# Performance work log

Hardware: AMD Instinct MI355X
Metric: run time of the kernel (lower is better)

Reference implementation:

```python
import jax, jax.numpy as jnp
import numpy as np

N, E, D = 50000, 800000, 128
BN_EPS = 1e-5
COORDS_WEIGHT = 1.0


def _p(key, shape, scale=0.05):
    return (jax.random.normal(key, shape, dtype=jnp.float32) * scale)


def setup_inputs() -> dict:
    key = jax.random.key(0)
    ks = jax.random.split(key, 16)
    inp = {
        "h": jax.random.normal(ks[0], (N, D), dtype=jnp.float32),
        "coord": jax.random.normal(ks[1], (N, 3), dtype=jnp.float32),
        "edge_index": jax.random.randint(ks[2], (2, E), 0, N, dtype=jnp.int32),
        # edge_mlp: Linear(2D+1 -> D), BN, ReLU, Linear(D -> D), BN, ReLU
        "e_w1": _p(ks[3], (D, 2 * D + 1)), "e_b1": jnp.zeros((D,), jnp.float32),
        "e_g1": jnp.ones((D,), jnp.float32), "e_be1": jnp.zeros((D,), jnp.float32),
        "e_w2": _p(ks[4], (D, D)), "e_b2": jnp.zeros((D,), jnp.float32),
        "e_g2": jnp.ones((D,), jnp.float32), "e_be2": jnp.zeros((D,), jnp.float32),
        # node_mlp: Linear(D + D -> D), BN, ReLU, Linear(D -> D)
        "n_w1": _p(ks[5], (D, 2 * D)), "n_b1": jnp.zeros((D,), jnp.float32),
        "n_g1": jnp.ones((D,), jnp.float32), "n_be1": jnp.zeros((D,), jnp.float32),
        "n_w2": _p(ks[6], (D, D)), "n_b2": jnp.zeros((D,), jnp.float32),
        # coord_mlp: Linear(D -> D), BN, ReLU, Linear(D -> 1, bias=False, tiny init)
        "c_w1": _p(ks[7], (D, D)), "c_b1": jnp.zeros((D,), jnp.float32),
        "c_g1": jnp.ones((D,), jnp.float32), "c_be1": jnp.zeros((D,), jnp.float32),
        "c_w2": _p(ks[8], (1, D), scale=0.001),
    }
    return inp


def _bn(x, g, b):
    # BatchNorm1d in training mode: biased batch stats over dim 0
    m = jnp.mean(x, axis=0)
    v = jnp.var(x, axis=0)
    return (x - m) * jax.lax.rsqrt(v + BN_EPS) * g + b


def _segment_mean(data, seg, num_segments):
    s = jax.ops.segment_sum(data, seg, num_segments=num_segments)
    c = jax.ops.segment_sum(jnp.ones((data.shape[0], 1), data.dtype), seg,
                            num_segments=num_segments)
    return s / jnp.maximum(c, 1.0)


def reference(h, coord, edge_index,
              e_w1, e_b1, e_g1, e_be1, e_w2, e_b2, e_g2, e_be2,
              n_w1, n_b1, n_g1, n_be1, n_w2, n_b2,
              c_w1, c_b1, c_g1, c_be1, c_w2):
    row, col = edge_index[0], edge_index[1]
    # coord2radial
    coord_diff = coord[row] - coord[col]                      # [E,3]
    radial = jnp.sum(coord_diff ** 2, axis=1, keepdims=True)  # [E,1]
    # edge_model
    e_in = jnp.concatenate([h[row], h[col], radial], axis=1)  # [E, 2D+1]
    x = jax.nn.relu(_bn(e_in @ e_w1.T + e_b1, e_g1, e_be1))
    edge_feat = jax.nn.relu(_bn(x @ e_w2.T + e_b2, e_g2, e_be2))  # [E,D]
    # coord_model
    y = jax.nn.relu(_bn(edge_feat @ c_w1.T + c_b1, c_g1, c_be1))
    scale = y @ c_w2.T                                        # [E,1]
    trans = jnp.clip(coord_diff * scale, -100.0, 100.0)
    coord_out = coord + _segment_mean(trans, row, coord.shape[0]) * COORDS_WEIGHT
    # node_model
    agg = _segment_mean(edge_feat, row, h.shape[0])           # [N,D]
    n_in = jnp.concatenate([h, agg], axis=1)                  # [N,2D]
    z = jax.nn.relu(_bn(n_in @ n_w1.T + n_b1, n_g1, n_be1))
    h_out = h + (z @ n_w2.T + n_b2)                           # recurrent residual
    return (h_out, coord_out)
```

## Files before the change

kernel.cpp:

```cpp
#include <hip/hip_runtime.h>

#define Nn 50000
#define En 800000
#define NSLOT 64

typedef __attribute__((ext_vector_type(8))) short short8;
typedef __attribute__((ext_vector_type(4))) float f32x4;

union U8 { uint4 u4; unsigned short us[8]; short8 s8; };

static __device__ __forceinline__ float bf2f(unsigned int lo16) {
  return __uint_as_float(lo16 << 16);
}
static __device__ __forceinline__ unsigned short f2bf(float f) {
  unsigned int x = __float_as_uint(f);
  return (unsigned short)((x + 0x7FFFu + ((x >> 16) & 1u)) >> 16);
}


__global__ __launch_bounds__(256) void k_prep_h(const float* __restrict__ h,
                                                unsigned short* __restrict__ nodeA) {
  int idx = blockIdx.x * 256 + threadIdx.x;
  if (idx >= Nn * 128) return;
  int n = idx >> 7, k = idx & 127;
  nodeA[(size_t)n * 256 + k] = f2bf(h[idx]);
}

__global__ __launch_bounds__(256) void k_prep_w(const float* __restrict__ src,
                                                unsigned short* __restrict__ dst, int Ksrc,
                                                int koff, int kshift, int total) {
  int idx = blockIdx.x * 256 + threadIdx.x;
  if (idx >= total) return;
  int n = idx >> kshift;
  int k = idx & ((1 << kshift) - 1);
  dst[idx] = f2bf(src[n * Ksrc + koff + k]);
}

__global__ void k_wlast(const float* __restrict__ e_w1, float* __restrict__ wlast) {
  int t = threadIdx.x;
  if (t < 128) wlast[t] = e_w1[t * 257 + 256];
}


__global__ __launch_bounds__(256) void k_count(const int* __restrict__ row, int* __restrict__ cnt) {
  int e = blockIdx.x * 256 + threadIdx.x;
  atomicAdd(&cnt[row[e]], 1);
}

__global__ __launch_bounds__(256) void k_fill(const int* __restrict__ row, int* __restrict__ cursor,
                                              int* __restrict__ elist) {
  int e = blockIdx.x * 256 + threadIdx.x;
  int pos = atomicAdd(&cursor[row[e]], 1);
  elist[pos] = e;
}

__global__ __launch_bounds__(1024) void k_scan(const int* __restrict__ cnt, int* __restrict__ start,
                                               int* __restrict__ cursor, int n) {
  __shared__ int wsum[16];
  __shared__ int carry;
  int tid = threadIdx.x, lane = tid & 63, wid = tid >> 6;
  if (tid == 0) carry = 0;
  __syncthreads();
  for (int base = 0; base < n; base += 1024) {
    int i = base + tid;
    int v = (i < n) ? cnt[i] : 0;
    int x = v;
#pragma unroll
    for (int d = 1; d < 64; d <<= 1) {
      int y = __shfl_up(x, d, 64);
      if (lane >= d) x += y;
    }
    if (lane == 63) wsum[wid] = x;
    __syncthreads();
    if (wid == 0) {
      int s = (lane < 16) ? wsum[lane] : 0;
#pragma unroll
      for (int d = 1; d < 16; d <<= 1) {
        int y = __shfl_up(s, d, 64);
        if (lane >= d) s += y;
      }
      if (lane < 16) wsum[lane] = s;
    }
    __syncthreads();
    int c0 = carry;
    int waveoff = (wid > 0) ? wsum[wid - 1] : 0;
    int incl = c0 + waveoff + x;
    if (i < n) {
      start[i] = incl - v;
      cursor[i] = incl - v;
    }
    __syncthreads();
    if (tid == 1023) carry = incl;
    __syncthreads();
  }
}


__global__ void k_fin(const float* __restrict__ statS, const float* __restrict__ statQ,
                      const float* __restrict__ g, const float* __restrict__ be, float invR,
                      float* __restrict__ bnS, float* __restrict__ bnSh) {
  int c = threadIdx.x;
  if (c >= 128) return;
  float s = 0.f, q = 0.f;
  for (int k = 0; k < NSLOT; ++k) {
    s += statS[k * 128 + c];
    q += statQ[k * 128 + c];
  }
  float mean = s * invR;
  float var = fmaxf(q * invR - mean * mean, 0.f);
  float rs = rsqrtf(var + 1e-5f);
  float sc = g[c] * rs;
  bnS[c] = sc;
  bnSh[c] = be[c] - mean * sc;
}

template <int KSTEPS, bool BN_A, bool STATS, bool FP32OUT>
__global__ __launch_bounds__(256) void k_gemmW(
    const unsigned short* __restrict__ A, int Astride ,
    const unsigned short* __restrict__ W , const float* __restrict__ bias,
    const float* __restrict__ bnS, const float* __restrict__ bnSh,
    unsigned short* __restrict__ outb, float* __restrict__ statS, float* __restrict__ statQ,
    const float* __restrict__ hres, float* __restrict__ outf, int R) {
  constexpr int K = KSTEPS * 32;
  constexpr int WST = K + 8;
  constexpr int SEGS = K / 8;
  __shared__ __align__(16) unsigned short smem[128 * WST];
  __shared__ float ssum[4][128], ssq[4][128];
  int tid = threadIdx.x;
  int w = tid >> 6, lane = tid & 63, m = lane & 15, kq = lane >> 4;
  int rbase = blockIdx.x * 128;
#pragma unroll
  for (int it = 0; it < SEGS / 2; ++it) {
    int idx = it * 256 + tid;
    int n = idx / SEGS, seg = idx % SEGS;
    uint4 v = *(const uint4*)(W + (size_t)n * K + seg * 8);
    *(uint4*)(smem + n * WST + seg * 8) = v;
  }
  __syncthreads();
  int row0 = rbase + w * 32 + m;
  int rc0 = min(row0, R - 1);
  int rc1 = min(row0 + 16, R - 1);
  f32x4 acc[2][8];
#pragma unroll
  for (int rt = 0; rt < 2; ++rt)
#pragma unroll
    for (int c = 0; c < 8; ++c) acc[rt][c] = (f32x4){0.f, 0.f, 0.f, 0.f};
#pragma unroll
  for (int ks = 0; ks < KSTEPS; ++ks) {
    int k0 = ks * 32 + kq * 8;
    U8 ua0, ua1;
    ua0.u4 = *(const uint4*)(A + (size_t)rc0 * Astride + k0);
    ua1.u4 = *(const uint4*)(A + (size_t)rc1 * Astride + k0);
    if (BN_A) {
      const float4* sp = (const float4*)(bnS + k0);
      const float4* hp = (const float4*)(bnSh + k0);
      float4 s0 = sp[0], s1 = sp[1], h0 = hp[0], h1 = hp[1];
      float sv[8] = {s0.x, s0.y, s0.z, s0.w, s1.x, s1.y, s1.z, s1.w};
      float hv[8] = {h0.x, h0.y, h0.z, h0.w, h1.x, h1.y, h1.z, h1.w};
#pragma unroll
      for (int j = 0; j < 8; ++j) {
        ua0.us[j] = f2bf(fmaxf(bf2f(ua0.us[j]) * sv[j] + hv[j], 0.f));
        ua1.us[j] = f2bf(fmaxf(bf2f(ua1.us[j]) * sv[j] + hv[j], 0.f));
      }
    }
#pragma unroll
    for (int c = 0; c < 8; ++c) {
      U8 ub;
      ub.u4 = *(const uint4*)(smem + (c * 16 + m) * WST + k0);
      acc[0][c] = __builtin_amdgcn_mfma_f32_16x16x32_bf16(ua0.s8, ub.s8, acc[0][c], 0, 0, 0);
      acc[1][c] = __builtin_amdgcn_mfma_f32_16x16x32_bf16(ua1.s8, ub.s8, acc[1][c], 0, 0, 0);
    }
  }
  if constexpr (FP32OUT) {
#pragma unroll
    for (int rt = 0; rt < 2; ++rt)
#pragma unroll
      for (int c = 0; c < 8; ++c) {
        int n = c * 16 + m;
        float bn_ = bias[n];
#pragma unroll
        for (int j = 0; j < 4; ++j) {
          int rr = rbase + w * 32 + rt * 16 + kq * 4 + j;
          if (rr < R) {
            size_t o = (size_t)rr * 128 + n;
            outf[o] = acc[rt][c][j] + bn_ + hres[o];
          }
        }
      }
  } else {
    __syncthreads();
    unsigned short* tile = smem;
#pragma unroll
    for (int c = 0; c < 8; ++c) {
      int n = c * 16 + m;
      float bn_ = bias ? bias[n] : 0.f;
      float s = 0.f, q = 0.f;
#pragma unroll
      for (int rt = 0; rt < 2; ++rt)
#pragma unroll
        for (int j = 0; j < 4; ++j) {
          int lr = w * 32 + rt * 16 + kq * 4 + j;
          float v = acc[rt][c][j] + bn_;
          tile[lr * 136 + n] = f2bf(v);
          if (STATS) {
            float sv = (rbase + lr < R) ? v : 0.f;
            s += sv;
            q = fmaf(sv, sv, q);
          }
        }
      if (STATS) {
        s += __shfl_xor(s, 16, 64); s += __shfl_xor(s, 32, 64);
        q += __shfl_xor(q, 16, 64); q += __shfl_xor(q, 32, 64);
        if (kq == 0) { ssum[w][n] = s; ssq[w][n] = q; }
      }
    }
    __syncthreads();
    const uint4* tl = (const uint4*)tile;
#pragma unroll
    for (int u = 0; u < 8; ++u) {
      int idx = u * 256 + tid;
      int rr = idx >> 4, seg = idx & 15;
      if (rbase + rr < R)
        *(uint4*)(outb + (size_t)(rbase + rr) * 128 + seg * 8) = tl[rr * 17 + seg];
    }
    if (STATS && tid < 128) {
      float s = ssum[0][tid] + ssum[1][tid] + ssum[2][tid] + ssum[3][tid];
      float q = ssq[0][tid] + ssq[1][tid] + ssq[2][tid] + ssq[3][tid];
      int slot = blockIdx.x & (NSLOT - 1);
      atomicAdd(&statS[slot * 128 + tid], s);
      atomicAdd(&statQ[slot * 128 + tid], q);
    }
  }
}

__global__ __launch_bounds__(256) void k_edge_comb(
    const unsigned short* __restrict__ hWr, const unsigned short* __restrict__ hWc,
    const float* __restrict__ coord, const int* __restrict__ rowp, const int* __restrict__ colp,
    const float* __restrict__ wlast, unsigned short* __restrict__ t,
    float* __restrict__ statS, float* __restrict__ statQ, int nwaves) {
  int tid = threadIdx.x, lane = tid & 63;
  int wid = blockIdx.x * 4 + (tid >> 6);
  int c2 = lane * 2;
  float wl0 = wlast[c2], wl1 = wlast[c2 + 1];
  float s0 = 0.f, s1 = 0.f, q0 = 0.f, q1 = 0.f;
  for (int e = wid; e < En; e += nwaves) {
    int r = rowp[e], c = colp[e];
    float dx = coord[r * 3 + 0] - coord[c * 3 + 0];
    float dy = coord[r * 3 + 1] - coord[c * 3 + 1];
    float dz = coord[r * 3 + 2] - coord[c * 3 + 2];
    float rad = dx * dx + dy * dy + dz * dz;
    unsigned int ua = *(const unsigned int*)(hWr + (size_t)r * 128 + c2);
    unsigned int ub = *(const unsigned int*)(hWc + (size_t)c * 128 + c2);
    float v0 = bf2f(ua & 0xFFFFu) + bf2f(ub & 0xFFFFu) + rad * wl0;
    float v1 = bf2f(ua >> 16) + bf2f(ub >> 16) + rad * wl1;
    *(unsigned int*)(t + (size_t)e * 128 + c2) = (unsigned)f2bf(v0) | ((unsigned)f2bf(v1) << 16);
    s0 += v0; q0 = fmaf(v0, v0, q0);
    s1 += v1; q1 = fmaf(v1, v1, q1);
  }
  int slot = wid & (NSLOT - 1);
  atomicAdd(&statS[slot * 128 + c2], s0);
  atomicAdd(&statS[slot * 128 + c2 + 1], s1);
  atomicAdd(&statQ[slot * 128 + c2], q0);
  atomicAdd(&statQ[slot * 128 + c2 + 1], q1);
}


__global__ __launch_bounds__(256) void k_scale(const unsigned short* __restrict__ t,
                                               const float* __restrict__ bnS,
                                               const float* __restrict__ bnSh,
                                               const float* __restrict__ cw2,
                                               float* __restrict__ scaleE) {
  int tid = threadIdx.x;
  int lane = tid & 63;
  long e = (long)blockIdx.x * 4 + (tid >> 6);
  int c2 = lane * 2;
  unsigned int u = *(const unsigned int*)(t + e * 128 + c2);
  float v0 = fmaxf(bf2f(u & 0xFFFFu) * bnS[c2] + bnSh[c2], 0.f);
  float v1 = fmaxf(bf2f(u >> 16) * bnS[c2 + 1] + bnSh[c2 + 1], 0.f);
  float p = v0 * cw2[c2] + v1 * cw2[c2 + 1];
#pragma unroll
  for (int d = 32; d; d >>= 1) p += __shfl_xor(p, d, 64);
  if (lane == 0) scaleE[e] = p;
}

__global__ __launch_bounds__(256) void k_agg(const unsigned short* __restrict__ t,
                                             const int* __restrict__ elist,
                                             const int* __restrict__ start,
                                             const int* __restrict__ cnt,
                                             const float* __restrict__ bnS,
                                             const float* __restrict__ bnSh,
                                             unsigned short* __restrict__ nodeA) {
  int tid = threadIdx.x;
  int lane = tid & 63;
  int n = blockIdx.x * 4 + (tid >> 6);
  if (n >= Nn) return;
  int deg = cnt[n], off = start[n];
  int c2 = lane * 2;
  float s0 = bnS[c2], s1 = bnS[c2 + 1], h0 = bnSh[c2], h1 = bnSh[c2 + 1];
  float a0 = 0.f, a1 = 0.f;
  for (int j = 0; j < deg; ++j) {
    int e = elist[off + j];
    unsigned int u = *(const unsigned int*)(t + (size_t)e * 128 + c2);
    a0 += fmaxf(bf2f(u & 0xFFFFu) * s0 + h0, 0.f);
    a1 += fmaxf(bf2f(u >> 16) * s1 + h1, 0.f);
  }
  float inv = 1.f / fmaxf((float)deg, 1.f);
  unsigned int o = (unsigned)f2bf(a0 * inv) | ((unsigned)f2bf(a1 * inv) << 16);
  *(unsigned int*)(nodeA + (size_t)n * 256 + 128 + c2) = o;
}

__global__ __launch_bounds__(256) void k_coord(const float* __restrict__ coord,
                                               const int* __restrict__ col,
                                               const int* __restrict__ elist,
                                               const int* __restrict__ start,
                                               const int* __restrict__ cnt,
                                               const float* __restrict__ scaleE,
                                               float* __restrict__ cout) {
  int tid = threadIdx.x;
  int lane = tid & 63;
  int n = blockIdx.x * 4 + (tid >> 6);
  if (n >= Nn) return;
  int deg = cnt[n], off = start[n];
  float cx0 = coord[n * 3 + 0], cy0 = coord[n * 3 + 1], cz0 = coord[n * 3 + 2];
  float ax = 0.f, ay = 0.f, az = 0.f;
  for (int j = lane; j < deg; j += 64) {
    int e = elist[off + j];
    int c = col[e];
    float s = scaleE[e];
    float tx = (cx0 - coord[c * 3 + 0]) * s;
    float ty = (cy0 - coord[c * 3 + 1]) * s;
    float tz = (cz0 - coord[c * 3 + 2]) * s;
    ax += fminf(fmaxf(tx, -100.f), 100.f);
    ay += fminf(fmaxf(ty, -100.f), 100.f);
    az += fminf(fmaxf(tz, -100.f), 100.f);
  }
#pragma unroll
  for (int d = 32; d; d >>= 1) {
    ax += __shfl_xor(ax, d, 64);
    ay += __shfl_xor(ay, d, 64);
    az += __shfl_xor(az, d, 64);
  }
  if (lane == 0) {
    float inv = 1.f / fmaxf((float)deg, 1.f);
    cout[n * 3 + 0] = cx0 + ax * inv;
    cout[n * 3 + 1] = cy0 + ay * inv;
    cout[n * 3 + 2] = cz0 + az * inv;
  }
}


extern "C" void kernel_launch(void* const* d_in, const int* in_sizes, int n_in, void* d_out,
                              int out_size, void* d_ws, size_t ws_size, hipStream_t stream) {
  (void)in_sizes; (void)n_in; (void)out_size; (void)ws_size;
  const float* h = (const float*)d_in[0];
  const float* coord = (const float*)d_in[1];
  const int* eidx = (const int*)d_in[2];
  const int* row = eidx;
  const int* col = eidx + En;
  const float* e_w1 = (const float*)d_in[3];
  const float* e_b1 = (const float*)d_in[4];
  const float* e_g1 = (const float*)d_in[5];
  const float* e_be1 = (const float*)d_in[6];
  const float* e_w2 = (const float*)d_in[7];
  const float* e_b2 = (const float*)d_in[8];
  const float* e_g2 = (const float*)d_in[9];
  const float* e_be2 = (const float*)d_in[10];
  const float* n_w1 = (const float*)d_in[11];
  const float* n_b1 = (const float*)d_in[12];
  const float* n_g1 = (const float*)d_in[13];
  const float* n_be1 = (const float*)d_in[14];
  const float* n_w2 = (const float*)d_in[15];
  const float* n_b2 = (const float*)d_in[16];
  const float* c_w1 = (const float*)d_in[17];
  const float* c_b1 = (const float*)d_in[18];
  const float* c_g1 = (const float*)d_in[19];
  const float* c_be1 = (const float*)d_in[20];
  const float* c_w2 = (const float*)d_in[21];

  char* base = (char*)d_ws;
  size_t off = 0;
  auto alloc = [&](size_t bytes) -> void* {
    void* p = base + off;
    off = (off + bytes + 255) & ~(size_t)255;
    return p;
  };
  unsigned short* t = (unsigned short*)alloc((size_t)En * 128 * 2);
  unsigned short* nodeA = (unsigned short*)alloc((size_t)Nn * 256 * 2);
  unsigned short* hWr = (unsigned short*)alloc((size_t)Nn * 128 * 2);
  unsigned short* hWc = (unsigned short*)alloc((size_t)Nn * 128 * 2);
  float* scaleE = (float*)alloc((size_t)En * 4);
  int* cnt = (int*)alloc((size_t)Nn * 4);
  int* startp = (int*)alloc((size_t)Nn * 4);
  int* cursor = (int*)alloc((size_t)Nn * 4);
  int* elist = (int*)alloc((size_t)En * 4);
  float* statS = (float*)alloc(4 * NSLOT * 128 * 4);
  float* statQ = (float*)alloc(4 * NSLOT * 128 * 4);
  float* bnS = (float*)alloc(4 * 128 * 4);
  float* bnSh = (float*)alloc(4 * 128 * 4);
  unsigned short* w1a = (unsigned short*)alloc(128 * 128 * 2);
  unsigned short* w1b = (unsigned short*)alloc(128 * 128 * 2);
  unsigned short* w2b = (unsigned short*)alloc(128 * 128 * 2);
  unsigned short* c1b = (unsigned short*)alloc(128 * 128 * 2);
  unsigned short* n1b = (unsigned short*)alloc(128 * 256 * 2);
  unsigned short* n2b = (unsigned short*)alloc(128 * 128 * 2);
  float* wlast = (float*)alloc(128 * 4);

  hipMemsetAsync(cnt, 0, (size_t)Nn * 4, stream);
  hipMemsetAsync(statS, 0, 4 * NSLOT * 128 * 4, stream);
  hipMemsetAsync(statQ, 0, 4 * NSLOT * 128 * 4, stream);

  k_prep_h<<<(Nn * 128 + 255) / 256, 256, 0, stream>>>(h, nodeA);
  k_prep_w<<<(128 * 128 + 255) / 256, 256, 0, stream>>>(e_w1, w1a, 257, 0, 7, 128 * 128);
  k_prep_w<<<(128 * 128 + 255) / 256, 256, 0, stream>>>(e_w1, w1b, 257, 128, 7, 128 * 128);
  k_prep_w<<<(128 * 128 + 255) / 256, 256, 0, stream>>>(e_w2, w2b, 128, 0, 7, 128 * 128);
  k_prep_w<<<(128 * 128 + 255) / 256, 256, 0, stream>>>(c_w1, c1b, 128, 0, 7, 128 * 128);
  k_prep_w<<<(128 * 256 + 255) / 256, 256, 0, stream>>>(n_w1, n1b, 256, 0, 8, 128 * 256);
  k_prep_w<<<(128 * 128 + 255) / 256, 256, 0, stream>>>(n_w2, n2b, 128, 0, 7, 128 * 128);
  k_wlast<<<1, 128, 0, stream>>>(e_w1, wlast);

  k_count<<<En / 256, 256, 0, stream>>>(row, cnt);
  k_scan<<<1, 1024, 0, stream>>>(cnt, startp, cursor, Nn);
  k_fill<<<En / 256, 256, 0, stream>>>(row, cursor, elist);

  const int gridN = (Nn + 127) / 128;
  k_gemmW<4, false, false, false><<<gridN, 256, 0, stream>>>(
      nodeA, 256, w1a, e_b1, nullptr, nullptr, hWr, nullptr, nullptr, nullptr, nullptr, Nn);
  k_gemmW<4, false, false, false><<<gridN, 256, 0, stream>>>(
      nodeA, 256, w1b, nullptr, nullptr, nullptr, hWc, nullptr, nullptr, nullptr, nullptr, Nn);

  k_edge_comb<<<1280, 256, 0, stream>>>(hWr, hWc, coord, row, col, wlast, t,
                                        statS + 0 * NSLOT * 128, statQ + 0 * NSLOT * 128,
                                        1280 * 4);
  k_fin<<<1, 128, 0, stream>>>(statS + 0 * NSLOT * 128, statQ + 0 * NSLOT * 128, e_g1, e_be1,
                               1.f / En, bnS + 0, bnSh + 0);

  k_gemmW<4, true, true, false><<<En / 128, 256, 0, stream>>>(
      t, 128, w2b, e_b2, bnS + 0, bnSh + 0, t, statS + 1 * NSLOT * 128, statQ + 1 * NSLOT * 128,
      nullptr, nullptr, En);
  k_fin<<<1, 128, 0, stream>>>(statS + 1 * NSLOT * 128, statQ + 1 * NSLOT * 128, e_g2, e_be2,
                               1.f / En, bnS + 128, bnSh + 128);

  k_agg<<<(Nn + 3) / 4, 256, 0, stream>>>(t, elist, startp, cnt, bnS + 128, bnSh + 128, nodeA);

  k_gemmW<4, true, true, false><<<En / 128, 256, 0, stream>>>(
      t, 128, c1b, c_b1, bnS + 128, bnSh + 128, t, statS + 2 * NSLOT * 128,
      statQ + 2 * NSLOT * 128, nullptr, nullptr, En);
  k_fin<<<1, 128, 0, stream>>>(statS + 2 * NSLOT * 128, statQ + 2 * NSLOT * 128, c_g1, c_be1,
                               1.f / En, bnS + 256, bnSh + 256);

  k_scale<<<En / 4, 256, 0, stream>>>(t, bnS + 256, bnSh + 256, c_w2, scaleE);
  float* hout = (float*)d_out;
  float* cout = hout + (size_t)Nn * 128;
  k_coord<<<(Nn + 3) / 4, 256, 0, stream>>>(coord, col, elist, startp, cnt, scaleE, cout);

  k_gemmW<8, false, true, false><<<gridN, 256, 0, stream>>>(
      nodeA, 256, n1b, n_b1, nullptr, nullptr, t, statS + 3 * NSLOT * 128,
      statQ + 3 * NSLOT * 128, nullptr, nullptr, Nn);
  k_fin<<<1, 128, 0, stream>>>(statS + 3 * NSLOT * 128, statQ + 3 * NSLOT * 128, n_g1, n_be1,
                               1.f / Nn, bnS + 384, bnSh + 384);
  k_gemmW<4, true, false, true><<<gridN, 256, 0, stream>>>(
      t, 128, n2b, n_b2, bnS + 384, bnSh + 384, nullptr, nullptr, nullptr, h, hout, Nn);
}
```

Measured before the change: 897.0 us.

## Sort edges by row, recompute first edge layer in GEMM, fuse coord MLP with aggregation

```diff
diff --git a/kernel.cpp b/kernel.cpp
--- a/kernel.cpp
+++ b/kernel.cpp
@@ -47,11 +47,16 @@
   atomicAdd(&cnt[row[e]], 1);
 }
 
-__global__ __launch_bounds__(256) void k_fill(const int* __restrict__ row, int* __restrict__ cursor,
-                                              int* __restrict__ elist) {
+__global__ __launch_bounds__(256) void k_fill(const int* __restrict__ row,
+                                              const int* __restrict__ col,
+                                              int* __restrict__ cursor,
+                                              unsigned short* __restrict__ rowS,
+                                              unsigned short* __restrict__ colS) {
   int e = blockIdx.x * 256 + threadIdx.x;
-  int pos = atomicAdd(&cursor[row[e]], 1);
-  elist[pos] = e;
+  int r = row[e];
+  int pos = atomicAdd(&cursor[r], 1);
+  rowS[pos] = (unsigned short)r;
+  colS[pos] = (unsigned short)col[e];
 }
 
 __global__ __launch_bounds__(1024) void k_scan(const int* __restrict__ cnt, int* __restrict__ start,
@@ -114,10 +119,10 @@
   bnSh[c] = be[c] - mean * sc;
 }
 
-template <int KSTEPS, bool BN_A, bool STATS, bool FP32OUT>
+template <int KSTEPS, bool BN_A, bool STATS, bool FP32OUT, bool STORE>
 __global__ __launch_bounds__(256) void k_gemmW(
-    const unsigned short* __restrict__ A, int Astride ,
-    const unsigned short* __restrict__ W , const float* __restrict__ bias,
+    const unsigned short* __restrict__ A, int Astride,
+    const unsigned short* __restrict__ W, const float* __restrict__ bias,
     const float* __restrict__ bnS, const float* __restrict__ bnSh,
     unsigned short* __restrict__ outb, float* __restrict__ statS, float* __restrict__ statQ,
     const float* __restrict__ hres, float* __restrict__ outf, int R) {
@@ -188,7 +193,7 @@
         }
       }
   } else {
-    __syncthreads();
+    if constexpr (STORE) __syncthreads();
     unsigned short* tile = smem;
 #pragma unroll
     for (int c = 0; c < 8; ++c) {
@@ -201,7 +206,7 @@
         for (int j = 0; j < 4; ++j) {
           int lr = w * 32 + rt * 16 + kq * 4 + j;
           float v = acc[rt][c][j] + bn_;
-          tile[lr * 136 + n] = f2bf(v);
+          if (STORE) tile[lr * 136 + n] = f2bf(v);
           if (STATS) {
             float sv = (rbase + lr < R) ? v : 0.f;
             s += sv;
@@ -214,46 +219,54 @@
         if (kq == 0) { ssum[w][n] = s; ssq[w][n] = q; }
       }
     }
-    __syncthreads();
-    const uint4* tl = (const uint4*)tile;
-#pragma unroll
-    for (int u = 0; u < 8; ++u) {
-      int idx = u * 256 + tid;
-      int rr = idx >> 4, seg = idx & 15;
-      if (rbase + rr < R)
-        *(uint4*)(outb + (size_t)(rbase + rr) * 128 + seg * 8) = tl[rr * 17 + seg];
-    }
-    if (STATS && tid < 128) {
-      float s = ssum[0][tid] + ssum[1][tid] + ssum[2][tid] + ssum[3][tid];
-      float q = ssq[0][tid] + ssq[1][tid] + ssq[2][tid] + ssq[3][tid];
-      int slot = blockIdx.x & (NSLOT - 1);
-      atomicAdd(&statS[slot * 128 + tid], s);
-      atomicAdd(&statQ[slot * 128 + tid], q);
-    }
-  }
-}
-
-__global__ __launch_bounds__(256) void k_edge_comb(
+    if constexpr (STORE) {
+      __syncthreads();
+      const uint4* tl = (const uint4*)tile;
+#pragma unroll
+      for (int u = 0; u < 8; ++u) {
+        int idx = u * 256 + tid;
+        int rr = idx >> 4, seg = idx & 15;
+        if (rbase + rr < R)
+          *(uint4*)(outb + (size_t)(rbase + rr) * 128 + seg * 8) = tl[rr * 17 + seg];
+      }
+    }
+    if (STATS) {
+      __syncthreads();
+      if (tid < 128) {
+        float s = ssum[0][tid] + ssum[1][tid] + ssum[2][tid] + ssum[3][tid];
+        float q = ssq[0][tid] + ssq[1][tid] + ssq[2][tid] + ssq[3][tid];
+        int slot = blockIdx.x & (NSLOT - 1);
+        atomicAdd(&statS[slot * 128 + tid], s);
+        atomicAdd(&statQ[slot * 128 + tid], q);
+      }
+    }
+  }
+}
+
+__global__ __launch_bounds__(256) void k_stats1(
     const unsigned short* __restrict__ hWr, const unsigned short* __restrict__ hWc,
-    const float* __restrict__ coord, const int* __restrict__ rowp, const int* __restrict__ colp,
-    const float* __restrict__ wlast, unsigned short* __restrict__ t,
-    float* __restrict__ statS, float* __restrict__ statQ, int nwaves) {
+    const float* __restrict__ coord, const unsigned short* __restrict__ rowS,
+    const unsigned short* __restrict__ colS, const float* __restrict__ wlast,
+    float* __restrict__ radS, float* __restrict__ statS, float* __restrict__ statQ,
+    int per_wave) {
   int tid = threadIdx.x, lane = tid & 63;
   int wid = blockIdx.x * 4 + (tid >> 6);
+  int e0 = wid * per_wave;
+  int e1 = min(e0 + per_wave, En);
   int c2 = lane * 2;
   float wl0 = wlast[c2], wl1 = wlast[c2 + 1];
   float s0 = 0.f, s1 = 0.f, q0 = 0.f, q1 = 0.f;
-  for (int e = wid; e < En; e += nwaves) {
-    int r = rowp[e], c = colp[e];
+  for (int e = e0; e < e1; ++e) {
+    int r = rowS[e], c = colS[e];
     float dx = coord[r * 3 + 0] - coord[c * 3 + 0];
     float dy = coord[r * 3 + 1] - coord[c * 3 + 1];
     float dz = coord[r * 3 + 2] - coord[c * 3 + 2];
     float rad = dx * dx + dy * dy + dz * dz;
+    if (lane == 0) radS[e] = rad;
     unsigned int ua = *(const unsigned int*)(hWr + (size_t)r * 128 + c2);
     unsigned int ub = *(const unsigned int*)(hWc + (size_t)c * 128 + c2);
     float v0 = bf2f(ua & 0xFFFFu) + bf2f(ub & 0xFFFFu) + rad * wl0;
     float v1 = bf2f(ua >> 16) + bf2f(ub >> 16) + rad * wl1;
-    *(unsigned int*)(t + (size_t)e * 128 + c2) = (unsigned)f2bf(v0) | ((unsigned)f2bf(v1) << 16);
     s0 += v0; q0 = fmaf(v0, v0, q0);
     s1 += v1; q1 = fmaf(v1, v1, q1);
   }
@@ -264,54 +277,209 @@
   atomicAdd(&statQ[slot * 128 + c2 + 1], q1);
 }
 
-
-__global__ __launch_bounds__(256) void k_scale(const unsigned short* __restrict__ t,
-                                               const float* __restrict__ bnS,
-                                               const float* __restrict__ bnSh,
-                                               const float* __restrict__ cw2,
-                                               float* __restrict__ scaleE) {
+__global__ __launch_bounds__(256) void k_egemm2(
+    const unsigned short* __restrict__ hWr, const unsigned short* __restrict__ hWc,
+    const float* __restrict__ radS, const unsigned short* __restrict__ rowS,
+    const unsigned short* __restrict__ colS, const unsigned short* __restrict__ W,
+    const float* __restrict__ bias, const float* __restrict__ wlast,
+    const float* __restrict__ bnS1, const float* __restrict__ bnSh1,
+    unsigned short* __restrict__ outb, float* __restrict__ statS, float* __restrict__ statQ) {
+  constexpr int WST = 136;
+  __shared__ __align__(16) unsigned short smem[128 * WST];
+  __shared__ float ssum[4][128], ssq[4][128];
   int tid = threadIdx.x;
-  int lane = tid & 63;
-  long e = (long)blockIdx.x * 4 + (tid >> 6);
-  int c2 = lane * 2;
-  unsigned int u = *(const unsigned int*)(t + e * 128 + c2);
-  float v0 = fmaxf(bf2f(u & 0xFFFFu) * bnS[c2] + bnSh[c2], 0.f);
-  float v1 = fmaxf(bf2f(u >> 16) * bnS[c2 + 1] + bnSh[c2 + 1], 0.f);
-  float p = v0 * cw2[c2] + v1 * cw2[c2 + 1];
-#pragma unroll
-  for (int d = 32; d; d >>= 1) p += __shfl_xor(p, d, 64);
-  if (lane == 0) scaleE[e] = p;
-}
-
-__global__ __launch_bounds__(256) void k_agg(const unsigned short* __restrict__ t,
-                                             const int* __restrict__ elist,
-                                             const int* __restrict__ start,
-                                             const int* __restrict__ cnt,
-                                             const float* __restrict__ bnS,
-                                             const float* __restrict__ bnSh,
-                                             unsigned short* __restrict__ nodeA) {
+  int w = tid >> 6, lane = tid & 63, m = lane & 15, kq = lane >> 4;
+  int rbase = blockIdx.x * 128;
+#pragma unroll
+  for (int it = 0; it < 8; ++it) {
+    int idx = it * 256 + tid;
+    int n = idx >> 4, seg = idx & 15;
+    uint4 v = *(const uint4*)(W + (size_t)n * 128 + seg * 8);
+    *(uint4*)(smem + n * WST + seg * 8) = v;
+  }
+  int rc0 = rbase + w * 32 + m, rc1 = rc0 + 16;
+  int r0 = rowS[rc0], c0 = colS[rc0];
+  int r1 = rowS[rc1], c1 = colS[rc1];
+  float rad0 = radS[rc0], rad1 = radS[rc1];
+  __syncthreads();
+  f32x4 acc[2][8];
+#pragma unroll
+  for (int rt = 0; rt < 2; ++rt)
+#pragma unroll
+    for (int c = 0; c < 8; ++c) acc[rt][c] = (f32x4){0.f, 0.f, 0.f, 0.f};
+#pragma unroll
+  for (int ks = 0; ks < 4; ++ks) {
+    int k0 = ks * 32 + kq * 8;
+    U8 a0r, a0c, a1r, a1c;
+    a0r.u4 = *(const uint4*)(hWr + (size_t)r0 * 128 + k0);
+    a0c.u4 = *(const uint4*)(hWc + (size_t)c0 * 128 + k0);
+    a1r.u4 = *(const uint4*)(hWr + (size_t)r1 * 128 + k0);
+    a1c.u4 = *(const uint4*)(hWc + (size_t)c1 * 128 + k0);
+    const float4* wp = (const float4*)(wlast + k0);
+    const float4* sp = (const float4*)(bnS1 + k0);
+    const float4* hp = (const float4*)(bnSh1 + k0);
+    float4 w0 = wp[0], w1 = wp[1], sA = sp[0], sB = sp[1], hA = hp[0], hB = hp[1];
+    float wv[8] = {w0.x, w0.y, w0.z, w0.w, w1.x, w1.y, w1.z, w1.w};
+    float sv[8] = {sA.x, sA.y, sA.z, sA.w, sB.x, sB.y, sB.z, sB.w};
+    float hv[8] = {hA.x, hA.y, hA.z, hA.w, hB.x, hB.y, hB.z, hB.w};
+    U8 ua0, ua1;
+#pragma unroll
+    for (int j = 0; j < 8; ++j) {
+      float v0 = bf2f(a0r.us[j]) + bf2f(a0c.us[j]) + rad0 * wv[j];
+      float v1 = bf2f(a1r.us[j]) + bf2f(a1c.us[j]) + rad1 * wv[j];
+      ua0.us[j] = f2bf(fmaxf(v0 * sv[j] + hv[j], 0.f));
+      ua1.us[j] = f2bf(fmaxf(v1 * sv[j] + hv[j], 0.f));
+    }
+#pragma unroll
+    for (int c = 0; c < 8; ++c) {
+      U8 ub;
+      ub.u4 = *(const uint4*)(smem + (c * 16 + m) * WST + k0);
+      acc[0][c] = __builtin_amdgcn_mfma_f32_16x16x32_bf16(ua0.s8, ub.s8, acc[0][c], 0, 0, 0);
+      acc[1][c] = __builtin_amdgcn_mfma_f32_16x16x32_bf16(ua1.s8, ub.s8, acc[1][c], 0, 0, 0);
+    }
+  }
+  __syncthreads();
+  unsigned short* tile = smem;
+#pragma unroll
+  for (int c = 0; c < 8; ++c) {
+    int n = c * 16 + m;
+    float bn_ = bias[n];
+    float s = 0.f, q = 0.f;
+#pragma unroll
+    for (int rt = 0; rt < 2; ++rt)
+#pragma unroll
+      for (int j = 0; j < 4; ++j) {
+        int lr = w * 32 + rt * 16 + kq * 4 + j;
+        float v = acc[rt][c][j] + bn_;
+        tile[lr * 136 + n] = f2bf(v);
+        s += v;
+        q = fmaf(v, v, q);
+      }
+    s += __shfl_xor(s, 16, 64); s += __shfl_xor(s, 32, 64);
+    q += __shfl_xor(q, 16, 64); q += __shfl_xor(q, 32, 64);
+    if (kq == 0) { ssum[w][n] = s; ssq[w][n] = q; }
+  }
+  __syncthreads();
+  const uint4* tl = (const uint4*)tile;
+#pragma unroll
+  for (int u = 0; u < 8; ++u) {
+    int idx = u * 256 + tid;
+    int rr = idx >> 4, seg = idx & 15;
+    *(uint4*)(outb + (size_t)(rbase + rr) * 128 + seg * 8) = tl[rr * 17 + seg];
+  }
+  if (tid < 128) {
+    float s = ssum[0][tid] + ssum[1][tid] + ssum[2][tid] + ssum[3][tid];
+    float q = ssq[0][tid] + ssq[1][tid] + ssq[2][tid] + ssq[3][tid];
+    int slot = blockIdx.x & (NSLOT - 1);
+    atomicAdd(&statS[slot * 128 + tid], s);
+    atomicAdd(&statQ[slot * 128 + tid], q);
+  }
+}
+
+__global__ __launch_bounds__(256) void k_c1agg(
+    const unsigned short* __restrict__ t, const unsigned short* __restrict__ W,
+    const float* __restrict__ bias, const float* __restrict__ bnS2,
+    const float* __restrict__ bnSh2, const float* __restrict__ bnS3,
+    const float* __restrict__ bnSh3, const float* __restrict__ cw2,
+    const unsigned short* __restrict__ rowS, float* __restrict__ aggAcc,
+    float* __restrict__ scaleE) {
+  __shared__ __align__(16) unsigned short smw[128 * 128];
+  __shared__ __align__(16) unsigned short ytile[128 * 128];
   int tid = threadIdx.x;
-  int lane = tid & 63;
-  int n = blockIdx.x * 4 + (tid >> 6);
-  if (n >= Nn) return;
-  int deg = cnt[n], off = start[n];
-  int c2 = lane * 2;
-  float s0 = bnS[c2], s1 = bnS[c2 + 1], h0 = bnSh[c2], h1 = bnSh[c2 + 1];
-  float a0 = 0.f, a1 = 0.f;
-  for (int j = 0; j < deg; ++j) {
-    int e = elist[off + j];
-    unsigned int u = *(const unsigned int*)(t + (size_t)e * 128 + c2);
-    a0 += fmaxf(bf2f(u & 0xFFFFu) * s0 + h0, 0.f);
-    a1 += fmaxf(bf2f(u >> 16) * s1 + h1, 0.f);
-  }
-  float inv = 1.f / fmaxf((float)deg, 1.f);
-  unsigned int o = (unsigned)f2bf(a0 * inv) | ((unsigned)f2bf(a1 * inv) << 16);
-  *(unsigned int*)(nodeA + (size_t)n * 256 + 128 + c2) = o;
+  int w = tid >> 6, lane = tid & 63, m = lane & 15, kq = lane >> 4;
+  int rbase = blockIdx.x * 128;
+#pragma unroll
+  for (int it = 0; it < 8; ++it) {
+    int idx = it * 256 + tid;
+    int n = idx >> 4, b = idx & 15;
+    uint4 v = *(const uint4*)(W + (size_t)n * 128 + b * 8);
+    *(uint4*)(smw + n * 128 + ((b ^ (n & 15)) << 3)) = v;
+  }
+  __syncthreads();
+  f32x4 acc[2][8];
+#pragma unroll
+  for (int rt = 0; rt < 2; ++rt)
+#pragma unroll
+    for (int c = 0; c < 8; ++c) acc[rt][c] = (f32x4){0.f, 0.f, 0.f, 0.f};
+  int r0l = w * 32 + m, r1l = r0l + 16;
+#pragma unroll
+  for (int ks = 0; ks < 4; ++ks) {
+    int k0 = ks * 32 + kq * 8;
+    int blk = ks * 4 + kq;
+    U8 ua0, ua1;
+    ua0.u4 = *(const uint4*)(t + (size_t)(rbase + r0l) * 128 + k0);
+    ua1.u4 = *(const uint4*)(t + (size_t)(rbase + r1l) * 128 + k0);
+    const float4* sp = (const float4*)(bnS2 + k0);
+    const float4* hp = (const float4*)(bnSh2 + k0);
+    float4 sA = sp[0], sB = sp[1], hA = hp[0], hB = hp[1];
+    float sv[8] = {sA.x, sA.y, sA.z, sA.w, sB.x, sB.y, sB.z, sB.w};
+    float hv[8] = {hA.x, hA.y, hA.z, hA.w, hB.x, hB.y, hB.z, hB.w};
+#pragma unroll
+    for (int j = 0; j < 8; ++j) {
+      ua0.us[j] = f2bf(fmaxf(bf2f(ua0.us[j]) * sv[j] + hv[j], 0.f));
+      ua1.us[j] = f2bf(fmaxf(bf2f(ua1.us[j]) * sv[j] + hv[j], 0.f));
+    }
+    *(uint4*)(ytile + r0l * 128 + ((blk ^ m) << 3)) = ua0.u4;
+    *(uint4*)(ytile + r1l * 128 + ((blk ^ m) << 3)) = ua1.u4;
+#pragma unroll
+    for (int c = 0; c < 8; ++c) {
+      U8 ub;
+      ub.u4 = *(const uint4*)(smw + (c * 16 + m) * 128 + ((blk ^ m) << 3));
+      acc[0][c] = __builtin_amdgcn_mfma_f32_16x16x32_bf16(ua0.s8, ub.s8, acc[0][c], 0, 0, 0);
+      acc[1][c] = __builtin_amdgcn_mfma_f32_16x16x32_bf16(ua1.s8, ub.s8, acc[1][c], 0, 0, 0);
+    }
+  }
+  float p[2][4] = {{0.f, 0.f, 0.f, 0.f}, {0.f, 0.f, 0.f, 0.f}};
+#pragma unroll
+  for (int c = 0; c < 8; ++c) {
+    int n = c * 16 + m;
+    float b1 = bias[n], s3 = bnS3[n], sh3 = bnSh3[n], w2 = cw2[n];
+#pragma unroll
+    for (int rt = 0; rt < 2; ++rt)
+#pragma unroll
+      for (int j = 0; j < 4; ++j) {
+        float t3v = acc[rt][c][j] + b1;
+        p[rt][j] += w2 * fmaxf(t3v * s3 + sh3, 0.f);
+      }
+  }
+#pragma unroll
+  for (int rt = 0; rt < 2; ++rt)
+#pragma unroll
+    for (int j = 0; j < 4; ++j) {
+      float v = p[rt][j];
+      v += __shfl_xor(v, 1, 64); v += __shfl_xor(v, 2, 64);
+      v += __shfl_xor(v, 4, 64); v += __shfl_xor(v, 8, 64);
+      if (m == 0) scaleE[rbase + w * 32 + rt * 16 + kq * 4 + j] = v;
+    }
+  __syncthreads();
+  int ch = tid & 127, half = tid >> 7;
+  int rlo = half * 64, rhi = rlo + 64;
+  int cur = rowS[rbase + rlo];
+  float run = 0.f;
+  for (int r = rlo; r < rhi; ++r) {
+    int nid = rowS[rbase + r];
+    if (nid != cur) {
+      atomicAdd(&aggAcc[(size_t)cur * 128 + ch], run);
+      run = 0.f;
+      cur = nid;
+    }
+    run += bf2f(ytile[r * 128 + (((ch >> 3) ^ (r & 15)) << 3) + (ch & 7)]);
+  }
+  atomicAdd(&aggAcc[(size_t)cur * 128 + ch], run);
+}
+
+__global__ __launch_bounds__(256) void k_aggfin(const float* __restrict__ aggAcc,
+                                                const int* __restrict__ cnt,
+                                                unsigned short* __restrict__ nodeA) {
+  int idx = blockIdx.x * 256 + threadIdx.x;
+  if (idx >= Nn * 128) return;
+  int n = idx >> 7, ch = idx & 127;
+  float inv = 1.f / fmaxf((float)cnt[n], 1.f);
+  nodeA[(size_t)n * 256 + 128 + ch] = f2bf(aggAcc[idx] * inv);
 }
 
 __global__ __launch_bounds__(256) void k_coord(const float* __restrict__ coord,
-                                               const int* __restrict__ col,
-                                               const int* __restrict__ elist,
+                                               const unsigned short* __restrict__ colS,
                                                const int* __restrict__ start,
                                                const int* __restrict__ cnt,
                                                const float* __restrict__ scaleE,
@@ -324,8 +492,8 @@
   float cx0 = coord[n * 3 + 0], cy0 = coord[n * 3 + 1], cz0 = coord[n * 3 + 2];
   float ax = 0.f, ay = 0.f, az = 0.f;
   for (int j = lane; j < deg; j += 64) {
-    int e = elist[off + j];
-    int c = col[e];
+    int e = off + j;
+    int c = colS[e];
     float s = scaleE[e];
     float tx = (cx0 - coord[c * 3 + 0]) * s;
     float ty = (cy0 - coord[c * 3 + 1]) * s;
@@ -388,11 +556,14 @@
   unsigned short* nodeA = (unsigned short*)alloc((size_t)Nn * 256 * 2);
   unsigned short* hWr = (unsigned short*)alloc((size_t)Nn * 128 * 2);
   unsigned short* hWc = (unsigned short*)alloc((size_t)Nn * 128 * 2);
+  float* aggAcc = (float*)hWr;
   float* scaleE = (float*)alloc((size_t)En * 4);
+  float* radS = scaleE;
+  unsigned short* rowS = (unsigned short*)alloc((size_t)En * 2);
+  unsigned short* colS = (unsigned short*)alloc((size_t)En * 2);
   int* cnt = (int*)alloc((size_t)Nn * 4);
   int* startp = (int*)alloc((size_t)Nn * 4);
   int* cursor = (int*)alloc((size_t)Nn * 4);
-  int* elist = (int*)alloc((size_t)En * 4);
   float* statS = (float*)alloc(4 * NSLOT * 128 * 4);
   float* statQ = (float*)alloc(4 * NSLOT * 128 * 4);
   float* bnS = (float*)alloc(4 * 128 * 4);
@@ -420,44 +591,47 @@
 
   k_count<<<En / 256, 256, 0, stream>>>(row, cnt);
   k_scan<<<1, 1024, 0, stream>>>(cnt, startp, cursor, Nn);
-  k_fill<<<En / 256, 256, 0, stream>>>(row, cursor, elist);
+  k_fill<<<En / 256, 256, 0, stream>>>(row, col, cursor, rowS, colS);
 
   const int gridN = (Nn + 127) / 128;
-  k_gemmW<4, false, false, false><<<gridN, 256, 0, stream>>>(
+  k_gemmW<4, false, false, false, true><<<gridN, 256, 0, stream>>>(
       nodeA, 256, w1a, e_b1, nullptr, nullptr, hWr, nullptr, nullptr, nullptr, nullptr, Nn);
-  k_gemmW<4, false, false, false><<<gridN, 256, 0, stream>>>(
+  k_gemmW<4, false, false, false, true><<<gridN, 256, 0, stream>>>(
       nodeA, 256, w1b, nullptr, nullptr, nullptr, hWc, nullptr, nullptr, nullptr, nullptr, Nn);
 
-  k_edge_comb<<<1280, 256, 0, stream>>>(hWr, hWc, coord, row, col, wlast, t,
-                                        statS + 0 * NSLOT * 128, statQ + 0 * NSLOT * 128,
-                                        1280 * 4);
+  const int per_wave = (En + 5119) / 5120;
+  k_stats1<<<1280, 256, 0, stream>>>(hWr, hWc, coord, rowS, colS, wlast, radS,
+                                     statS + 0 * NSLOT * 128, statQ + 0 * NSLOT * 128, per_wave);
   k_fin<<<1, 128, 0, stream>>>(statS + 0 * NSLOT * 128, statQ + 0 * NSLOT * 128, e_g1, e_be1,
                                1.f / En, bnS + 0, bnSh + 0);
 
-  k_gemmW<4, true, true, false><<<En / 128, 256, 0, stream>>>(
-      t, 128, w2b, e_b2, bnS + 0, bnSh + 0, t, statS + 1 * NSLOT * 128, statQ + 1 * NSLOT * 128,
-      nullptr, nullptr, En);
+  k_egemm2<<<En / 128, 256, 0, stream>>>(hWr, hWc, radS, rowS, colS, w2b, e_b2, wlast, bnS + 0,
+                                         bnSh + 0, t, statS + 1 * NSLOT * 128,
+                                         statQ + 1 * NSLOT * 128);
   k_fin<<<1, 128, 0, stream>>>(statS + 1 * NSLOT * 128, statQ + 1 * NSLOT * 128, e_g2, e_be2,
                                1.f / En, bnS + 128, bnSh + 128);
 
-  k_agg<<<(Nn + 3) / 4, 256, 0, stream>>>(t, elist, startp, cnt, bnS + 128, bnSh + 128, nodeA);
-
-  k_gemmW<4, true, true, false><<<En / 128, 256, 0, stream>>>(
-      t, 128, c1b, c_b1, bnS + 128, bnSh + 128, t, statS + 2 * NSLOT * 128,
+  hipMemsetAsync(aggAcc, 0, (size_t)Nn * 128 * 4, stream);
+
+  k_gemmW<4, true, true, false, false><<<En / 128, 256, 0, stream>>>(
+      t, 128, c1b, c_b1, bnS + 128, bnSh + 128, nullptr, statS + 2 * NSLOT * 128,
       statQ + 2 * NSLOT * 128, nullptr, nullptr, En);
   k_fin<<<1, 128, 0, stream>>>(statS + 2 * NSLOT * 128, statQ + 2 * NSLOT * 128, c_g1, c_be1,
                                1.f / En, bnS + 256, bnSh + 256);
 
-  k_scale<<<En / 4, 256, 0, stream>>>(t, bnS + 256, bnSh + 256, c_w2, scaleE);
+  k_c1agg<<<En / 128, 256, 0, stream>>>(t, c1b, c_b1, bnS + 128, bnSh + 128, bnS + 256,
+                                        bnSh + 256, c_w2, rowS, aggAcc, scaleE);
+  k_aggfin<<<(Nn * 128 + 255) / 256, 256, 0, stream>>>(aggAcc, cnt, nodeA);
+
   float* hout = (float*)d_out;
   float* cout = hout + (size_t)Nn * 128;
-  k_coord<<<(Nn + 3) / 4, 256, 0, stream>>>(coord, col, elist, startp, cnt, scaleE, cout);
-
-  k_gemmW<8, false, true, false><<<gridN, 256, 0, stream>>>(
+  k_coord<<<(Nn + 3) / 4, 256, 0, stream>>>(coord, colS, startp, cnt, scaleE, cout);
+
+  k_gemmW<8, false, true, false, true><<<gridN, 256, 0, stream>>>(
       nodeA, 256, n1b, n_b1, nullptr, nullptr, t, statS + 3 * NSLOT * 128,
       statQ + 3 * NSLOT * 128, nullptr, nullptr, Nn);
   k_fin<<<1, 128, 0, stream>>>(statS + 3 * NSLOT * 128, statQ + 3 * NSLOT * 128, n_g1, n_be1,
                                1.f / Nn, bnS + 384, bnSh + 384);
-  k_gemmW<4, true, false, true><<<gridN, 256, 0, stream>>>(
+  k_gemmW<4, true, false, true, true><<<gridN, 256, 0, stream>>>(
       t, 128, n2b, n_b2, bnS + 384, bnSh + 384, nullptr, nullptr, nullptr, h, hout, Nn);
 }
```

New measurement: 958.3 us. +6.8%, slower.
